# Kernel optimization log

Measured on AMD Instinct MI355X. Metric: run time of the kernel, lower is better.

Reference implementation:

```python
import jax, jax.numpy as jnp
import numpy as np

B, S, D, H = 4, 2048, 512, 8
DH = D // H


def setup_inputs() -> dict:
    key = jax.random.key(0)
    ks = jax.random.split(key, 6)
    embeddings = jax.random.normal(ks[0], (B, S, D), dtype=jnp.float32)
    token_masks = jax.random.randint(ks[1], (B, S), 0, 2, dtype=jnp.int32)
    # keras 'random_normal' initializer: stddev 0.05
    Wq = 0.05 * jax.random.normal(ks[2], (D, D), dtype=jnp.float32)
    Wk = 0.05 * jax.random.normal(ks[3], (D, D), dtype=jnp.float32)
    Wv = 0.05 * jax.random.normal(ks[4], (D, D), dtype=jnp.float32)
    Wo = 0.05 * jax.random.normal(ks[5], (D, D), dtype=jnp.float32)
    return {"embeddings": embeddings, "token_masks": token_masks,
            "Wq": Wq, "Wk": Wk, "Wv": Wv, "Wo": Wo}


def reference(embeddings, token_masks, Wq, Wk, Wv, Wo):
    b, s, d = embeddings.shape
    h, dh = H, d // H
    # QKV projections -> (b, h, s, dh)
    def split_heads(x):
        return x.reshape(b, s, h, dh).transpose(0, 2, 1, 3)
    Q = split_heads(embeddings @ Wq)
    K = split_heads(embeddings @ Wk)
    V = split_heads(embeddings @ Wv)
    scores = jnp.einsum('bhqd,bhkd->bhqk', Q, K) / jnp.sqrt(jnp.float32(dh))
    # causal (lower-triangular) mask combined with padding mask on both q and k
    causal = jnp.tril(jnp.ones((s, s), dtype=jnp.float32))
    tm = token_masks.astype(jnp.float32)
    attn_mask = causal[None, None, :, :] * tm[:, None, None, :] * tm[:, None, :, None]
    scores = jnp.where(attn_mask > 0, scores, jnp.float32(-1e30))
    weights = jax.nn.softmax(scores, axis=-1)  # dropout omitted (inference/eval mode)
    context = jnp.einsum('bhqk,bhkd->bhqd', weights, V)
    context = context.transpose(0, 2, 1, 3).reshape(b, s, d)
    return context @ Wo
```

## Files before the change

kernel.cpp:

```cpp
#include <hip/hip_runtime.h>
#include <hip/hip_bf16.h>
#include <stdint.h>

#define BATCH 4
#define SEQ 2048
#define DMODEL 512
#define NHEAD 8
#define HD 64

#define C1 0.18033688f
#define BIAS2 -23.0831207f

using f32x4 = __attribute__((ext_vector_type(4))) float;
using bfrag = __attribute__((ext_vector_type(8))) short;

__device__ __forceinline__ short f2bf(float f) {
  uint32_t x = __builtin_bit_cast(uint32_t, f);
  uint32_t r = (x + 0x7fffu + ((x >> 16) & 1u)) >> 16;
  return (short)r;
}
__device__ __forceinline__ short f2bf_fast(float f) {
  return (short)((__builtin_bit_cast(uint32_t, f) + 0x8000u) >> 16);
}
__device__ __forceinline__ float bf2f(short s) {
  return __builtin_bit_cast(float, ((uint32_t)(uint16_t)s) << 16);
}
__device__ __forceinline__ void gl_lds16(const void* g, void* l) {
  __builtin_amdgcn_global_load_lds(
      (const __attribute__((address_space(1))) void*)g,
      (__attribute__((address_space(3))) void*)l, 16, 0, 0);
}
__device__ __forceinline__ bool sniff_f32(const void* p, int tid) {
  const uint32_t* xw = (const uint32_t*)p;
  const int lane = tid & 63;
  const uint32_t w1 = xw[lane], w2 = xw[64 + lane];
  bool bad = (((w1 >> 7) & 0xffu) >= 0xB0u) | (((w1 >> 23) & 0xffu) >= 0xB0u) |
             (((w2 >> 7) & 0xffu) >= 0xB0u) | (((w2 >> 23) & 0xffu) >= 0xB0u);
  return __ballot(bad) != 0ull;
}

__global__ __launch_bounds__(256) void prep(const void* __restrict__ X,
                                            const void* __restrict__ w0,
                                            const void* __restrict__ w1,
                                            const void* __restrict__ w2,
                                            const void* __restrict__ w3,
                                            short* __restrict__ Xb,
                                            short* __restrict__ wtAll,
                                            float* __restrict__ mv) {
  const int blk = blockIdx.x, tid = threadIdx.x;
  if (blk < 2048) {
    const bool isf32 = sniff_f32(X, tid);
    const int i = (blk * 256 + tid) * 8;
    if (isf32) {
      const float* f = (const float*)X;
      short r[8];
#pragma unroll
      for (int j = 0; j < 8; ++j) r[j] = f2bf(f[i + j]);
      *(bfrag*)&Xb[i] = *(bfrag*)r;
    } else {
      *(bfrag*)&Xb[i] = *(const bfrag*)&((const short*)X)[i];
    }
  } else if (blk < 3072) {
    __shared__ short t[32][33];
    const int idx = blk - 2048;
    const int z = idx >> 8, rem = idx & 255;
    const void* in = (z == 0) ? w0 : (z == 1) ? w1 : (z == 2) ? w2 : w3;
    short* out = wtAll + (size_t)z * DMODEL * DMODEL;
    const int tx = tid & 31, ty = tid >> 5;
    const bool isf32 = sniff_f32(in, tid);
    const int n0 = (rem & 15) * 32, k0 = (rem >> 4) * 32;
#pragma unroll
    for (int i = ty; i < 32; i += 8) {
      const int idx2 = (k0 + i) * DMODEL + n0 + tx;
      t[i][tx] = isf32 ? f2bf(((const float*)in)[idx2]) : ((const short*)in)[idx2];
    }
    __syncthreads();
#pragma unroll
    for (int i = ty; i < 32; i += 8) out[(n0 + i) * DMODEL + k0 + tx] = t[tx][i];
  } else {
#pragma unroll
    for (int j = 0; j < 8; ++j) mv[tid * 8 + j] = 0.f;
  }
}

__global__ __launch_bounds__(256) void gemm_qkv(const short* __restrict__ X,
                                                const short* __restrict__ WtAll,
                                                short* __restrict__ Qo,
                                                short* __restrict__ Ko,
                                                short* __restrict__ Vo,
                                                float* __restrict__ mv) {
  __shared__ __align__(16) short As[128 * 32];
  __shared__ __align__(16) short Bs[128 * 32];
  const int which = blockIdx.z;
  const short* Wt = WtAll + which * DMODEL * DMODEL;
  const int m0 = blockIdx.y * 128, n0 = blockIdx.x * 128;
  const int tid = threadIdx.x, lane = tid & 63, wave = tid >> 6;
  const int l15 = lane & 15, quad = lane >> 4;
  const int wm = wave >> 1, wn = wave & 1;
  const int lrow = lane >> 2, lcol = (lane & 3) * 8;
  f32x4 acc[4][4] = {};
  for (int kc = 0; kc < DMODEL; kc += 32) {
#pragma unroll
    for (int i = 0; i < 2; ++i) {
      const int r0 = (wave * 2 + i) * 16;
      gl_lds16(&X[(size_t)(m0 + r0 + lrow) * DMODEL + kc + lcol], &As[r0 * 32]);
      gl_lds16(&Wt[(size_t)(n0 + r0 + lrow) * DMODEL + kc + lcol], &Bs[r0 * 32]);
    }
    __syncthreads();
    bfrag a[4], b[4];
#pragma unroll
    for (int t = 0; t < 4; ++t) {
      a[t] = *(const bfrag*)&As[(wm * 64 + t * 16 + l15) * 32 + quad * 8];
      b[t] = *(const bfrag*)&Bs[(wn * 64 + t * 16 + l15) * 32 + quad * 8];
    }
#pragma unroll
    for (int tm = 0; tm < 4; ++tm)
#pragma unroll
      for (int tn = 0; tn < 4; ++tn)
        acc[tm][tn] = __builtin_amdgcn_mfma_f32_16x16x32_bf16(a[tm], b[tn], acc[tm][tn], 0, 0, 0);
    __syncthreads();
  }
  short* O = (which == 0) ? Qo : (which == 1) ? Ko : Vo;
#pragma unroll
  for (int tn = 0; tn < 4; ++tn) {
    const int col = n0 + wn * 64 + tn * 16 + l15;
    const int h = col >> 6, d = col & 63;
#pragma unroll
    for (int tm = 0; tm < 4; ++tm) {
#pragma unroll
      for (int r = 0; r < 4; ++r) {
        const int row = m0 + wm * 64 + tm * 16 + quad * 4 + r;
        const int b = row >> 11, s = row & 2047;
        O[((b * NHEAD + h) * SEQ + s) * HD + d] = f2bf(acc[tm][tn][r]);
      }
    }
  }
  if (which == 2) {
    const int b = (m0 + wm * 64) >> 11;
#pragma unroll
    for (int tn = 0; tn < 4; ++tn) {
      float s = 0.f;
#pragma unroll
      for (int tm = 0; tm < 4; ++tm)
#pragma unroll
        for (int r = 0; r < 4; ++r) s += acc[tm][tn][r];
      s += __shfl_xor(s, 16);
      s += __shfl_xor(s, 32);
      if (quad == 0) {
        const int col = n0 + wn * 64 + tn * 16 + l15;
        const int h = col >> 6, d = col & 63;
        atomicAdd(&mv[(b * NHEAD + h) * 64 + d], s);
      }
    }
  }
}

__global__ __launch_bounds__(256) void gemm_out(const short* __restrict__ X,
                                                const short* __restrict__ Wt,
                                                float* __restrict__ O) {
  __shared__ __align__(16) short As[128 * 32];
  __shared__ __align__(16) short Bs[128 * 32];
  const int m0 = blockIdx.y * 128, n0 = blockIdx.x * 128;
  const int tid = threadIdx.x, lane = tid & 63, wave = tid >> 6;
  const int l15 = lane & 15, quad = lane >> 4;
  const int wm = wave >> 1, wn = wave & 1;
  const int lrow = lane >> 2, lcol = (lane & 3) * 8;
  f32x4 acc[4][4] = {};
  for (int kc = 0; kc < DMODEL; kc += 32) {
#pragma unroll
    for (int i = 0; i < 2; ++i) {
      const int r0 = (wave * 2 + i) * 16;
      gl_lds16(&X[(size_t)(m0 + r0 + lrow) * DMODEL + kc + lcol], &As[r0 * 32]);
      gl_lds16(&Wt[(size_t)(n0 + r0 + lrow) * DMODEL + kc + lcol], &Bs[r0 * 32]);
    }
    __syncthreads();
    bfrag a[4], b[4];
#pragma unroll
    for (int t = 0; t < 4; ++t) {
      a[t] = *(const bfrag*)&As[(wm * 64 + t * 16 + l15) * 32 + quad * 8];
      b[t] = *(const bfrag*)&Bs[(wn * 64 + t * 16 + l15) * 32 + quad * 8];
    }
#pragma unroll
    for (int tm = 0; tm < 4; ++tm)
#pragma unroll
      for (int tn = 0; tn < 4; ++tn)
        acc[tm][tn] = __builtin_amdgcn_mfma_f32_16x16x32_bf16(a[tm], b[tn], acc[tm][tn], 0, 0, 0);
    __syncthreads();
  }
#pragma unroll
  for (int tm = 0; tm < 4; ++tm)
#pragma unroll
    for (int tn = 0; tn < 4; ++tn) {
      const int col = n0 + wn * 64 + tn * 16 + l15;
#pragma unroll
      for (int r = 0; r < 4; ++r) {
        const int row = m0 + wm * 64 + tm * 16 + quad * 4 + r;
        O[(size_t)row * DMODEL + col] = acc[tm][tn][r];
      }
    }
}

__global__ __launch_bounds__(256, 4) void attn(const short* __restrict__ Q,
                                               const short* __restrict__ K,
                                               const short* __restrict__ V,
                                               const int* __restrict__ tmask,
                                               const float* __restrict__ meanV,
                                               short* __restrict__ ctx) {
  __shared__ __align__(16) short Ks[64 * 72];
  __shared__ __align__(16) short Vts[64 * 64];
  __shared__ __align__(16) short Ps[4 * 16 * 64];
  __shared__ int tmq[64];
  __shared__ int tmk[64];
  const int m2 = blockIdx.x >> 3, a3 = blockIdx.x & 7;
  const int j2 = blockIdx.y >> 3, b3 = blockIdx.y & 7;
  const int quart = (m2 + j2) & 3;
  const int qi = quart * 8 + ((quart & 1) ? (7 - a3) : a3);
  const int bh = j2 * 8 + b3;
  const int b = bh >> 3, h = bh & 7;
  const int q0 = qi * 64;
  const int tid = threadIdx.x, lane = tid & 63, wave = tid >> 6;
  const int l15 = lane & 15, quad = lane >> 4;
  const size_t base = (size_t)bh * SEQ * HD;

  bfrag qa0 = *(const bfrag*)&Q[base + (size_t)(q0 + wave * 16 + l15) * HD + quad * 8];
  bfrag qa1 = *(const bfrag*)&Q[base + (size_t)(q0 + wave * 16 + l15) * HD + 32 + quad * 8];
  if (tid < 64) tmq[tid] = tmask[b * SEQ + q0 + tid];

  f32x4 accO[4] = {};
  float lrow[4] = {0.f, 0.f, 0.f, 0.f};

  const int rp = tid >> 3, sgp = tid & 7;
  bfrag kA, kB, vA, vB;
  int tmreg = 0;

  auto prefetch = [&](int kc) {
    const size_t o0 = base + (size_t)(kc + 2 * rp) * HD + sgp * 8;
    kA = *(const bfrag*)&K[o0];
    kB = *(const bfrag*)&K[o0 + HD];
    vA = *(const bfrag*)&V[o0];
    vB = *(const bfrag*)&V[o0 + HD];
    if (tid < 64) tmreg = tmask[b * SEQ + kc + tid];
  };
  auto store_lds = [&]() {
    *(bfrag*)&Ks[(2 * rp) * 72 + sgp * 8] = kA;
    *(bfrag*)&Ks[(2 * rp + 1) * 72 + sgp * 8] = kB;
    const int g = ((rp >> 2) ^ sgp) & 7;
    const int kpos = (2 * rp) & 7;
#pragma unroll
    for (int j = 0; j < 8; ++j) {
      const uint32_t w = (uint32_t)(uint16_t)vA[j] | ((uint32_t)(uint16_t)vB[j] << 16);
      *(uint32_t*)&Vts[(sgp * 8 + j) * 64 + g * 8 + kpos] = w;
    }
    if (tid < 64) tmk[tid] = tmreg;
  };
  auto compute = [&](bool diag) {
    f32x4 sacc[4] = {};
#pragma unroll
    for (int t = 0; t < 4; ++t) {
      bfrag b0 = *(const bfrag*)&Ks[(t * 16 + l15) * 72 + quad * 8];
      sacc[t] = __builtin_amdgcn_mfma_f32_16x16x32_bf16(qa0, b0, sacc[t], 0, 0, 0);
    }
#pragma unroll
    for (int t = 0; t < 4; ++t) {
      bfrag b1 = *(const bfrag*)&Ks[(t * 16 + l15) * 72 + 32 + quad * 8];
      sacc[t] = __builtin_amdgcn_mfma_f32_16x16x32_bf16(qa1, b1, sacc[t], 0, 0, 0);
    }
    float badd[4];
#pragma unroll
    for (int t = 0; t < 4; ++t) badd[t] = tmk[t * 16 + l15] ? BIAS2 : -1e30f;
#pragma unroll
    for (int r = 0; r < 4; ++r) {
      const int m = quad * 4 + r;
#pragma unroll
      for (int t = 0; t < 4; ++t) {
        float p = exp2f(fmaf(sacc[t][r], C1, badd[t]));
        if (diag && (t * 16 + l15 > wave * 16 + m)) p = 0.f;
        lrow[r] += p;
        const int g = ((t * 2 + (l15 >> 3)) ^ (m & 7) ^ ((m >> 3) << 1)) & 7;
        Ps[wave * 1024 + m * 64 + g * 8 + (l15 & 7)] = f2bf_fast(p);
      }
    }
#pragma unroll
    for (int ks = 0; ks < 2; ++ks) {
#pragma unroll
      for (int t = 0; t < 4; ++t) {
        const int gp = ((ks * 4 + quad) ^ (l15 & 7) ^ ((l15 >> 3) << 1)) & 7;
        bfrag pa = *(const bfrag*)&Ps[wave * 1024 + l15 * 64 + gp * 8];
        const int d = t * 16 + l15;
        const int gv = ((ks * 4 + quad) ^ (d >> 3)) & 7;
        bfrag vb = *(const bfrag*)&Vts[d * 64 + gv * 8];
        accO[t] = __builtin_amdgcn_mfma_f32_16x16x32_bf16(pa, vb, accO[t], 0, 0, 0);
      }
    }
  };

  prefetch(0);
  for (int kc = 0; kc <= q0; kc += 64) {
    __syncthreads();
    store_lds();
    __syncthreads();
    if (kc < q0) prefetch(kc + 64);
    compute(kc == q0);
  }

#pragma unroll
  for (int r = 0; r < 4; ++r) {
    float l = lrow[r];
    l += __shfl_xor(l, 1);
    l += __shfl_xor(l, 2);
    l += __shfl_xor(l, 4);
    l += __shfl_xor(l, 8);
    lrow[r] = 1.f / l;
  }
  const int qrow_loc = wave * 16 + quad * 4;
#pragma unroll
  for (int t = 0; t < 4; ++t) {
    const int d = t * 16 + l15;
    const float mvd = meanV[bh * 64 + d] * (1.f / 2048.f);
#pragma unroll
    for (int r = 0; r < 4; ++r) {
      const int row = qrow_loc + r;
      float val = accO[t][r] * lrow[r];
      if (tmq[row] == 0) val = mvd;
      ctx[((size_t)(b * SEQ + q0 + row)) * DMODEL + h * HD + d] = f2bf(val);
    }
  }
}

extern "C" void kernel_launch(void* const* d_in, const int* in_sizes, int n_in,
                              void* d_out, int out_size, void* d_ws, size_t ws_size,
                              hipStream_t stream) {
  const void* X = d_in[0];
  const int* tmask = (const int*)d_in[1];
  const void* Wq = d_in[2];
  const void* Wk = d_in[3];
  const void* Wv = d_in[4];
  const void* Wo = d_in[5];
  float* out = (float*)d_out;
  char* ws = (char*)d_ws;

  const size_t WELEM = (size_t)DMODEL * DMODEL;
  const size_t TELEM = (size_t)BATCH * NHEAD * SEQ * HD;

  float* mv = (float*)(ws + 4096);
  short* wt = (short*)(ws + 4096 + 8192);
  short* Xb = (short*)(ws + 4096 + 8192 + 2097152);
  short* Qb = Xb + TELEM;
  short* Kb = Qb + TELEM;
  short* Vb = Kb + TELEM;
  short* Cb = Vb + TELEM;

  prep<<<3073, 256, 0, stream>>>(X, Wq, Wk, Wv, Wo, Xb, wt, mv);
  gemm_qkv<<<dim3(4, 64, 3), 256, 0, stream>>>(Xb, wt, Qb, Kb, Vb, mv);
  attn<<<dim3(32, 32), 256, 0, stream>>>(Qb, Kb, Vb, tmask, mv, Cb);
  gemm_out<<<dim3(4, 64), 256, 0, stream>>>(Cb, wt + 3 * WELEM, out);
}
```

Measured before the change: 177.3 us.

## Process two 64-row query tiles per attention block to reuse K/V tiles

Each attention block now handles 128 query rows as two 64-row sub-tiles that share every loaded K/V chunk, halving K/V global loads and LDS staging per query row. The grid shrinks to 16x32 blocks with a simpler reversed-order mapping for load balance, and launch bounds drop to 2 blocks per SM for the extra registers. The V-transpose and P swizzles are also reworked to suit the doubled P buffer. The cost is fewer blocks, lower occupancy, and extra masked work on the diagonal chunk for the first sub-tile.

```diff
diff --git a/kernel.cpp b/kernel.cpp
--- a/kernel.cpp
+++ b/kernel.cpp
@@ -200,7 +200,7 @@
     }
 }
 
-__global__ __launch_bounds__(256, 4) void attn(const short* __restrict__ Q,
+__global__ __launch_bounds__(256, 2) void attn(const short* __restrict__ Q,
                                                const short* __restrict__ K,
                                                const short* __restrict__ V,
                                                const int* __restrict__ tmask,
@@ -208,26 +208,27 @@
                                                short* __restrict__ ctx) {
   __shared__ __align__(16) short Ks[64 * 72];
   __shared__ __align__(16) short Vts[64 * 64];
-  __shared__ __align__(16) short Ps[4 * 16 * 64];
-  __shared__ int tmq[64];
+  __shared__ __align__(16) short Ps[4 * 32 * 64];
+  __shared__ int tmq[128];
   __shared__ int tmk[64];
-  const int m2 = blockIdx.x >> 3, a3 = blockIdx.x & 7;
-  const int j2 = blockIdx.y >> 3, b3 = blockIdx.y & 7;
-  const int quart = (m2 + j2) & 3;
-  const int qi = quart * 8 + ((quart & 1) ? (7 - a3) : a3);
-  const int bh = j2 * 8 + b3;
+  const int qi = (blockIdx.y < 16) ? blockIdx.x : (15 - blockIdx.x);
+  const int bh = blockIdx.y;
   const int b = bh >> 3, h = bh & 7;
-  const int q0 = qi * 64;
+  const int q0 = qi * 128;
   const int tid = threadIdx.x, lane = tid & 63, wave = tid >> 6;
   const int l15 = lane & 15, quad = lane >> 4;
   const size_t base = (size_t)bh * SEQ * HD;
 
-  bfrag qa0 = *(const bfrag*)&Q[base + (size_t)(q0 + wave * 16 + l15) * HD + quad * 8];
-  bfrag qa1 = *(const bfrag*)&Q[base + (size_t)(q0 + wave * 16 + l15) * HD + 32 + quad * 8];
-  if (tid < 64) tmq[tid] = tmask[b * SEQ + q0 + tid];
-
-  f32x4 accO[4] = {};
-  float lrow[4] = {0.f, 0.f, 0.f, 0.f};
+  const size_t qrow0 = base + (size_t)(q0 + wave * 16 + l15) * HD;
+  const size_t qrow1 = qrow0 + (size_t)64 * HD;
+  bfrag qa00 = *(const bfrag*)&Q[qrow0 + quad * 8];
+  bfrag qa01 = *(const bfrag*)&Q[qrow0 + 32 + quad * 8];
+  bfrag qa10 = *(const bfrag*)&Q[qrow1 + quad * 8];
+  bfrag qa11 = *(const bfrag*)&Q[qrow1 + 32 + quad * 8];
+  if (tid < 128) tmq[tid] = tmask[b * SEQ + q0 + tid];
+
+  f32x4 accO0[4] = {}, accO1[4] = {};
+  float lr0[4] = {0.f, 0.f, 0.f, 0.f}, lr1[4] = {0.f, 0.f, 0.f, 0.f};
 
   const int rp = tid >> 3, sgp = tid & 7;
   bfrag kA, kB, vA, vB;
@@ -244,7 +245,7 @@
   auto store_lds = [&]() {
     *(bfrag*)&Ks[(2 * rp) * 72 + sgp * 8] = kA;
     *(bfrag*)&Ks[(2 * rp + 1) * 72 + sgp * 8] = kB;
-    const int g = ((rp >> 2) ^ sgp) & 7;
+    const int g = ((rp >> 2) ^ ((sgp & 1) << 2) ^ (sgp >> 1)) & 7;
     const int kpos = (2 * rp) & 7;
 #pragma unroll
     for (int j = 0; j < 8; ++j) {
@@ -253,76 +254,105 @@
     }
     if (tid < 64) tmk[tid] = tmreg;
   };
-  auto compute = [&](bool diag) {
-    f32x4 sacc[4] = {};
+
+  prefetch(0);
+  for (int kc = 0; kc <= q0 + 64; kc += 64) {
+    __syncthreads();
+    store_lds();
+    __syncthreads();
+    if (kc <= q0) prefetch(kc + 64);
+    const bool live0 = (kc <= q0);
+    const bool dg0 = (kc == q0);
+    const bool dg1 = (kc == q0 + 64);
+
+    f32x4 sa[4] = {}, sb[4] = {};
 #pragma unroll
     for (int t = 0; t < 4; ++t) {
       bfrag b0 = *(const bfrag*)&Ks[(t * 16 + l15) * 72 + quad * 8];
-      sacc[t] = __builtin_amdgcn_mfma_f32_16x16x32_bf16(qa0, b0, sacc[t], 0, 0, 0);
-    }
-#pragma unroll
-    for (int t = 0; t < 4; ++t) {
+      sa[t] = __builtin_amdgcn_mfma_f32_16x16x32_bf16(qa00, b0, sa[t], 0, 0, 0);
+      sb[t] = __builtin_amdgcn_mfma_f32_16x16x32_bf16(qa10, b0, sb[t], 0, 0, 0);
       bfrag b1 = *(const bfrag*)&Ks[(t * 16 + l15) * 72 + 32 + quad * 8];
-      sacc[t] = __builtin_amdgcn_mfma_f32_16x16x32_bf16(qa1, b1, sacc[t], 0, 0, 0);
+      sa[t] = __builtin_amdgcn_mfma_f32_16x16x32_bf16(qa01, b1, sa[t], 0, 0, 0);
+      sb[t] = __builtin_amdgcn_mfma_f32_16x16x32_bf16(qa11, b1, sb[t], 0, 0, 0);
     }
     float badd[4];
 #pragma unroll
     for (int t = 0; t < 4; ++t) badd[t] = tmk[t * 16 + l15] ? BIAS2 : -1e30f;
+
+    if (live0) {
+#pragma unroll
+      for (int r = 0; r < 4; ++r) {
+        const int m = quad * 4 + r;
+#pragma unroll
+        for (int t = 0; t < 4; ++t) {
+          float p = exp2f(fmaf(sa[t][r], C1, badd[t]));
+          if (dg0 && (t * 16 + l15 > wave * 16 + m)) p = 0.f;
+          lr0[r] += p;
+          const int g = ((t * 2 + (l15 >> 3)) ^ (m & 7) ^ ((m >> 3) << 1)) & 7;
+          Ps[wave * 2048 + m * 64 + g * 8 + (l15 & 7)] = f2bf_fast(p);
+        }
+      }
+    }
 #pragma unroll
     for (int r = 0; r < 4; ++r) {
       const int m = quad * 4 + r;
 #pragma unroll
       for (int t = 0; t < 4; ++t) {
-        float p = exp2f(fmaf(sacc[t][r], C1, badd[t]));
-        if (diag && (t * 16 + l15 > wave * 16 + m)) p = 0.f;
-        lrow[r] += p;
-        const int g = ((t * 2 + (l15 >> 3)) ^ (m & 7) ^ ((m >> 3) << 1)) & 7;
-        Ps[wave * 1024 + m * 64 + g * 8 + (l15 & 7)] = f2bf_fast(p);
-      }
-    }
+        float p = exp2f(fmaf(sb[t][r], C1, badd[t]));
+        if (dg1 && (t * 16 + l15 > wave * 16 + m)) p = 0.f;
+        lr1[r] += p;
+        const int g = ((t * 2 + (l15 >> 3)) ^ (m & 7) ^ (((m >> 3) << 1) ^ 4)) & 7;
+        Ps[wave * 2048 + (16 + m) * 64 + g * 8 + (l15 & 7)] = f2bf_fast(p);
+      }
+    }
+
 #pragma unroll
     for (int ks = 0; ks < 2; ++ks) {
+      const int gp0 = ((ks * 4 + quad) ^ (l15 & 7) ^ ((l15 >> 3) << 1)) & 7;
+      const int gp1 = gp0 ^ 4;
+      bfrag pa0 = *(const bfrag*)&Ps[wave * 2048 + l15 * 64 + gp0 * 8];
+      bfrag pa1 = *(const bfrag*)&Ps[wave * 2048 + (16 + l15) * 64 + gp1 * 8];
 #pragma unroll
       for (int t = 0; t < 4; ++t) {
-        const int gp = ((ks * 4 + quad) ^ (l15 & 7) ^ ((l15 >> 3) << 1)) & 7;
-        bfrag pa = *(const bfrag*)&Ps[wave * 1024 + l15 * 64 + gp * 8];
         const int d = t * 16 + l15;
-        const int gv = ((ks * 4 + quad) ^ (d >> 3)) & 7;
+        const int gv = ((ks * 4 + quad) ^ ((l15 >> 3) << 2) ^ t) & 7;
         bfrag vb = *(const bfrag*)&Vts[d * 64 + gv * 8];
-        accO[t] = __builtin_amdgcn_mfma_f32_16x16x32_bf16(pa, vb, accO[t], 0, 0, 0);
-      }
-    }
-  };
-
-  prefetch(0);
-  for (int kc = 0; kc <= q0; kc += 64) {
-    __syncthreads();
-    store_lds();
-    __syncthreads();
-    if (kc < q0) prefetch(kc + 64);
-    compute(kc == q0);
+        if (live0) accO0[t] = __builtin_amdgcn_mfma_f32_16x16x32_bf16(pa0, vb, accO0[t], 0, 0, 0);
+        accO1[t] = __builtin_amdgcn_mfma_f32_16x16x32_bf16(pa1, vb, accO1[t], 0, 0, 0);
+      }
+    }
   }
 
 #pragma unroll
   for (int r = 0; r < 4; ++r) {
-    float l = lrow[r];
+    float l = lr0[r];
     l += __shfl_xor(l, 1);
     l += __shfl_xor(l, 2);
     l += __shfl_xor(l, 4);
     l += __shfl_xor(l, 8);
-    lrow[r] = 1.f / l;
-  }
-  const int qrow_loc = wave * 16 + quad * 4;
+    lr0[r] = 1.f / l;
+    float l2 = lr1[r];
+    l2 += __shfl_xor(l2, 1);
+    l2 += __shfl_xor(l2, 2);
+    l2 += __shfl_xor(l2, 4);
+    l2 += __shfl_xor(l2, 8);
+    lr1[r] = 1.f / l2;
+  }
+  const int qrl = wave * 16 + quad * 4;
 #pragma unroll
   for (int t = 0; t < 4; ++t) {
     const int d = t * 16 + l15;
     const float mvd = meanV[bh * 64 + d] * (1.f / 2048.f);
 #pragma unroll
     for (int r = 0; r < 4; ++r) {
-      const int row = qrow_loc + r;
-      float val = accO[t][r] * lrow[r];
-      if (tmq[row] == 0) val = mvd;
-      ctx[((size_t)(b * SEQ + q0 + row)) * DMODEL + h * HD + d] = f2bf(val);
+      const int row0 = qrl + r;
+      float v0 = accO0[t][r] * lr0[r];
+      if (tmq[row0] == 0) v0 = mvd;
+      ctx[((size_t)(b * SEQ + q0 + row0)) * DMODEL + h * HD + d] = f2bf(v0);
+      const int row1 = 64 + qrl + r;
+      float v1 = accO1[t][r] * lr1[r];
+      if (tmq[row1] == 0) v1 = mvd;
+      ctx[((size_t)(b * SEQ + q0 + row1)) * DMODEL + h * HD + d] = f2bf(v1);
     }
   }
 }
@@ -352,6 +382,6 @@
 
   prep<<<3073, 256, 0, stream>>>(X, Wq, Wk, Wv, Wo, Xb, wt, mv);
   gemm_qkv<<<dim3(4, 64, 3), 256, 0, stream>>>(Xb, wt, Qb, Kb, Vb, mv);
-  attn<<<dim3(32, 32), 256, 0, stream>>>(Qb, Kb, Vb, tmask, mv, Cb);
+  attn<<<dim3(16, 32), 256, 0, stream>>>(Qb, Kb, Vb, tmask, mv, Cb);
   gemm_out<<<dim3(4, 64), 256, 0, stream>>>(Cb, wt + 3 * WELEM, out);
 }
```

New measurement: 187.9 us. +6.0%, slower.
